# Optimization experiments

Measured on AMD Instinct MI355X. Metric: run time of the kernel, lower is better.

## Reference

```python
import jax, jax.numpy as jnp
import numpy as np

N = 50000
E = 800000
IN_C = 128
HID = 128
OUT_C = 64
HEADS = 8
HD1 = HID // HEADS   # 16 per-head dim, layer 1 (concat)
HD2 = OUT_C          # 64 per-head dim, layer 2 (concat=False, mean over heads)
NEG_SLOPE = 0.2


def setup_inputs() -> dict:
    key = jax.random.key(0)
    ks = jax.random.split(key, 12)
    x = jax.random.normal(ks[0], (N, IN_C), dtype=jnp.float32)
    edge_index = jax.random.randint(ks[1], (2, E), 0, N, dtype=jnp.int64)
    s1 = 1.0 / np.sqrt(IN_C)
    s2 = 1.0 / np.sqrt(HID)
    W1 = jax.random.normal(ks[2], (IN_C, HEADS * HD1), dtype=jnp.float32) * s1
    att_src1 = jax.random.normal(ks[3], (HEADS, HD1), dtype=jnp.float32) * s1
    att_dst1 = jax.random.normal(ks[4], (HEADS, HD1), dtype=jnp.float32) * s1
    b1 = jnp.zeros((HID,), dtype=jnp.float32)
    W2 = jax.random.normal(ks[5], (HID, HEADS * HD2), dtype=jnp.float32) * s2
    att_src2 = jax.random.normal(ks[6], (HEADS, HD2), dtype=jnp.float32) * s2
    att_dst2 = jax.random.normal(ks[7], (HEADS, HD2), dtype=jnp.float32) * s2
    b2 = jnp.zeros((OUT_C,), dtype=jnp.float32)
    return {"x": x, "edge_index": edge_index,
            "W1": W1, "att_src1": att_src1, "att_dst1": att_dst1, "b1": b1,
            "W2": W2, "att_src2": att_src2, "att_dst2": att_dst2, "b2": b2}


def _gat_conv(x, W, a_src, a_dst, bias, src, dst, heads, head_dim, concat):
    n = x.shape[0]
    h = (x @ W).reshape(n, heads, head_dim)                      # [N,H,D]
    alpha_s = jnp.einsum('nhd,hd->nh', h, a_src)                  # [N,H]
    alpha_d = jnp.einsum('nhd,hd->nh', h, a_dst)                  # [N,H]
    e = jax.nn.leaky_relu(alpha_s[src] + alpha_d[dst], NEG_SLOPE)  # [E,H]
    # segment softmax over edges grouped by destination node
    m = jax.ops.segment_max(e, dst, num_segments=n)               # [N,H]
    m = jnp.where(jnp.isfinite(m), m, 0.0)
    ex = jnp.exp(e - m[dst])
    denom = jax.ops.segment_sum(ex, dst, num_segments=n)
    alpha = ex / (denom[dst] + 1e-16)                             # [E,H]
    out = jax.ops.segment_sum(h[src] * alpha[:, :, None], dst, num_segments=n)  # [N,H,D]
    if concat:
        out = out.reshape(n, heads * head_dim)
    else:
        out = out.mean(axis=1)
    return out + bias


def reference(x, edge_index, W1, att_src1, att_dst1, b1, W2, att_src2, att_dst2, b2):
    # PyG GATConv default add_self_loops=True
    loops = jnp.arange(N, dtype=edge_index.dtype)
    src = jnp.concatenate([edge_index[0], loops])
    dst = jnp.concatenate([edge_index[1], loops])
    h = _gat_conv(x, W1, att_src1, att_dst1, b1, src, dst, HEADS, HD1, True)
    h = jax.nn.relu(h)
    out = _gat_conv(h, W2, att_src2, att_dst2, b2, src, dst, HEADS, HD2, False)
    return out
```

## Files before the change

kernel.cpp:

```cpp
#include <hip/hip_runtime.h>

#define N_NODES 50000
#define N_EDGES 800000
#define ET (N_EDGES + N_NODES)
#define HEADS 8
#define NPAD 50048
#define SCAN_NB 196
#define CAP 96
#define LRS 1032

typedef __attribute__((ext_vector_type(8))) _Float16 half8;
typedef __attribute__((ext_vector_type(2))) _Float16 half2v;
typedef __attribute__((ext_vector_type(4))) float f32x4;

__device__ __forceinline__ void wave_lds_fence(){
  asm volatile("s_waitcnt lgkmcnt(0)" ::: "memory");
}

__device__ __forceinline__ int edge_src(const int* ei, int e, int is64){
  if (e >= N_EDGES) return e - N_EDGES;
  return is64 ? ei[2*e] : ei[e];
}
__device__ __forceinline__ int edge_dst(const int* ei, int e, int is64){
  if (e >= N_EDGES) return e - N_EDGES;
  return is64 ? ei[2*(N_EDGES + e)] : ei[N_EDGES + e];
}

__global__ void k_init(const int* __restrict__ ei, int* __restrict__ deg,
                       int* __restrict__ cnt, int* __restrict__ flag){
  int i = blockIdx.x*blockDim.x + threadIdx.x;
  if (i < N_NODES){ deg[i] = 0; cnt[i] = 0; }
  if (i == 0){
    int zeros = 0;
    for (int k = 0; k < 64; k++){
      if (ei[2*k + 1] == 0) zeros++;
    }
    *flag = (zeros >= 60) ? 1 : 0;
  }
}

__global__ void k_degree(const int* __restrict__ ei, int* __restrict__ deg,
                         const int* __restrict__ flag){
  int e = blockIdx.x*blockDim.x + threadIdx.x;
  if (e >= ET) return;
  int is64 = *flag;
  int d = edge_dst(ei, e, is64);
  atomicAdd(&deg[d], 1);
}

__global__ void k_scan_part(const int* __restrict__ deg, int* __restrict__ loc,
                            int* __restrict__ part, int* __restrict__ hist_blk){
  __shared__ int lds[256];
  __shared__ int hl[256];
  int t = threadIdx.x, i = blockIdx.x*256 + t;
  int v = (i < N_NODES) ? deg[i] : 0;
  hl[t] = 0;
  __syncthreads();
  if (i < N_NODES){
    int b = v > 255 ? 255 : v;
    atomicAdd(&hl[255 - b], 1);
  }
  lds[t] = v;
  __syncthreads();
  for (int off = 1; off < 256; off <<= 1){
    int x = (t >= off) ? lds[t - off] : 0;
    __syncthreads();
    lds[t] += x;
    __syncthreads();
  }
  if (i < N_NODES) loc[i] = lds[t] - v;
  if (t == 255) part[blockIdx.x] = lds[255];
  hist_blk[t*SCAN_NB + blockIdx.x] = hl[t];
}

__global__ void k_scan_carry(int* __restrict__ part, int* __restrict__ carry,
                             int* __restrict__ hist_blk){
  __shared__ int lds[256];
  int t = threadIdx.x;
  int v = (t < SCAN_NB) ? part[t] : 0;
  lds[t] = v;
  __syncthreads();
  for (int off = 1; off < 256; off <<= 1){
    int x = (t >= off) ? lds[t - off] : 0;
    __syncthreads();
    lds[t] += x;
    __syncthreads();
  }
  if (t < SCAN_NB) carry[t] = lds[t] - v;
  __syncthreads();
  int tot = 0;
  for (int b = 0; b < SCAN_NB; b++) tot += hist_blk[t*SCAN_NB + b];
  lds[t] = tot;
  __syncthreads();
  for (int off = 1; off < 256; off <<= 1){
    int x = (t >= off) ? lds[t - off] : 0;
    __syncthreads();
    lds[t] += x;
    __syncthreads();
  }
  int run = lds[t] - tot;
  for (int b = 0; b < SCAN_NB; b++){
    int c = hist_blk[t*SCAN_NB + b];
    hist_blk[t*SCAN_NB + b] = run;
    run += c;
  }
}

__global__ void k_scan_add(const int* __restrict__ loc, const int* __restrict__ carry,
                           int* __restrict__ row_ptr, const int* __restrict__ deg,
                           const int* __restrict__ hist_blk, int* __restrict__ perm){
  __shared__ int hl[256];
  int t = threadIdx.x, i = blockIdx.x*256 + t;
  hl[t] = 0;
  __syncthreads();
  if (i < N_NODES){
    row_ptr[i] = loc[i] + carry[i >> 8];
    int d = deg[i]; if (d > 255) d = 255;
    int bin = 255 - d;
    int rank = atomicAdd(&hl[bin], 1);
    perm[hist_blk[bin*SCAN_NB + blockIdx.x] + rank] = i;
  }
  if (i == 0) row_ptr[N_NODES] = ET;
}

__global__ void k_fill(const int* __restrict__ ei, const int* __restrict__ row_ptr,
                       int* __restrict__ cnt, int* __restrict__ col,
                       const int* __restrict__ flag){
  int e = blockIdx.x*blockDim.x + threadIdx.x;
  if (e >= ET) return;
  int is64 = *flag;
  int s = edge_src(ei, e, is64);
  int d = edge_dst(ei, e, is64);
  int pos = atomicAdd(&cnt[d], 1);
  col[row_ptr[d] + pos] = s;
}

__global__ void k_wprep(const float* __restrict__ W1, const float* __restrict__ W2,
                        const float* __restrict__ as2, const float* __restrict__ ad2,
                        _Float16* __restrict__ Bp1, _Float16* __restrict__ Bp,
                        float* __restrict__ ws2, float* __restrict__ wd2){
  int b = blockIdx.x;
  int t_ = threadIdx.x;
  if (b < 256){
    int t = b*256 + t_;
    int j = t & 7, lane = (t >> 3) & 63, nt = (t >> 9) & 3, kt = t >> 11;
    int k = kt*32 + (lane >> 4)*8 + j;
    int c = nt*16 + (lane & 15);
    int h = k >> 7, kk = k & 127;
    Bp[t] = (_Float16)(0.125f * W2[kk*512 + h*64 + c]);
  } else if (b < 320){
    int t = (b - 256)*256 + t_;
    int j = t & 7, lane = (t >> 3) & 63, nt = (t >> 9) & 7, kt = t >> 12;
    int k = kt*32 + (lane >> 4)*8 + j;
    int c = nt*16 + (lane & 15);
    Bp1[t] = (_Float16)W1[k*128 + c];
  } else {
    int t = (b - 320)*256 + t_;
    int k = t >> 3, h = t & 7;
    float s = 0.f, d = 0.f;
    for (int dd = 0; dd < 64; dd++){
      float w = W2[k*512 + h*64 + dd];
      s += w * as2[h*64 + dd];
      d += w * ad2[h*64 + dd];
    }
    ws2[h*128 + k] = s;
    wd2[h*128 + k] = d;
  }
}

__global__ void __launch_bounds__(256) k_gemm1_mfma(
    const float* __restrict__ x, const _Float16* __restrict__ Bp1,
    _Float16* __restrict__ h1,
    const float* __restrict__ as1, const float* __restrict__ ad1,
    float* __restrict__ als1, float* __restrict__ ald1){
  int tid = threadIdx.x;
  int lane = tid & 63, wv = tid >> 6;
  int n0 = blockIdx.x*64 + wv*16;
  int rowA = n0 + (lane & 15);
  int koff = (lane >> 4)*8;
  const float* xr = x + (size_t)rowA*128 + koff;
  f32x4 acc[8];
  #pragma unroll
  for (int i = 0; i < 8; i++) acc[i] = (f32x4){0.f,0.f,0.f,0.f};
  bool inb = (rowA < N_NODES);
  #pragma unroll
  for (int kt = 0; kt < 4; kt++){
    half8 af;
    if (inb){
      float4 a0 = *(const float4*)(xr + kt*32);
      float4 a1 = *(const float4*)(xr + kt*32 + 4);
      af = (half8){(_Float16)a0.x,(_Float16)a0.y,(_Float16)a0.z,(_Float16)a0.w,
                   (_Float16)a1.x,(_Float16)a1.y,(_Float16)a1.z,(_Float16)a1.w};
    } else {
      af = (half8){0,0,0,0,0,0,0,0};
    }
    #pragma unroll
    for (int nt = 0; nt < 8; nt++){
      half8 bf = *(const half8*)(Bp1 + (((kt*8 + nt)*64 + lane) << 3));
      acc[nt] = __builtin_amdgcn_mfma_f32_16x16x32_f16(af, bf, acc[nt], 0, 0, 0);
    }
  }
  int m = lane & 15, q = lane >> 4;
  int r0 = n0 + q*4;
  #pragma unroll
  for (int nt = 0; nt < 8; nt++){
    int c = nt*16 + m;
    #pragma unroll
    for (int r = 0; r < 4; r++){
      int n = r0 + r;
      if (n < N_NODES) h1[(size_t)n*128 + c] = (_Float16)acc[nt][r];
    }
  }
  float as1v[8], ad1v[8];
  #pragma unroll
  for (int nt = 0; nt < 8; nt++){
    as1v[nt] = as1[nt*16 + m];
    ad1v[nt] = ad1[nt*16 + m];
  }
  #pragma unroll
  for (int r = 0; r < 4; r++){
    float vs[8], vd[8];
    #pragma unroll
    for (int nt = 0; nt < 8; nt++){
      vs[nt] = acc[nt][r]*as1v[nt];
      vd[nt] = acc[nt][r]*ad1v[nt];
      #pragma unroll
      for (int off = 1; off < 16; off <<= 1){
        vs[nt] += __shfl_xor(vs[nt], off, 64);
        vd[nt] += __shfl_xor(vd[nt], off, 64);
      }
    }
    int n = r0 + r;
    if (m == r && n < N_NODES){
      float4 v0; v0.x = vs[0]; v0.y = vs[1]; v0.z = vs[2]; v0.w = vs[3];
      float4 v1; v1.x = vs[4]; v1.y = vs[5]; v1.z = vs[6]; v1.w = vs[7];
      float4 w0; w0.x = vd[0]; w0.y = vd[1]; w0.z = vd[2]; w0.w = vd[3];
      float4 w1; w1.x = vd[4]; w1.y = vd[5]; w1.z = vd[6]; w1.w = vd[7];
      *(float4*)&als1[n*8]     = v0;
      *(float4*)&als1[n*8 + 4] = v1;
      *(float4*)&ald1[n*8]     = w0;
      *(float4*)&ald1[n*8 + 4] = w1;
    }
  }
}

__global__ void k_attn_agg1(const _Float16* __restrict__ h1,
    const float* __restrict__ als, const float* __restrict__ ald,
    const int* __restrict__ row_ptr, const int* __restrict__ col,
    const float* __restrict__ bias, _Float16* __restrict__ hr,
    const float* __restrict__ ws2, const float* __restrict__ wd2,
    float* __restrict__ als2, float* __restrict__ ald2,
    const int* __restrict__ perm){
  __shared__ _Float16 ew_s[4][CAP*8];
  __shared__ int col_s[4][CAP];
  __shared__ _Float16 ot_s[4][132];
  int tid = threadIdx.x;
  int wv = tid >> 6, lane = tid & 63;
  int n = perm[blockIdx.x*4 + wv];
  int beg = row_ptr[n], end = row_ptr[n+1];
  int deg = end - beg;
  int items = deg*8;
  int h = lane & 7;
  float ad = ald[n*8 + h];
  _Float16* es = ew_s[wv];
  int* cs = col_s[wv];
  float l = 0.f;
  int itc = items < CAP*8 ? items : CAP*8;
  int it = lane;
  for (; it < itc; it += 64){
    int e = it >> 3;
    int s = col[beg + e];
    float a = als[s*8 + h] + ad;
    a = (a > 0.f) ? a : 0.2f*a;
    float ex = __expf(a);
    es[it] = (_Float16)ex;
    if ((it & 7) == 0) cs[e] = s;
    l += ex;
  }
  for (; it < items; it += 64){
    int s = col[beg + (it >> 3)];
    float a = als[s*8 + h] + ad;
    a = (a > 0.f) ? a : 0.2f*a;
    l += __expf(a);
  }
  l += __shfl_xor(l, 8, 64);
  l += __shfl_xor(l, 16, 64);
  l += __shfl_xor(l, 32, 64);
  float inv = 1.f / (l + 1e-16f);
  wave_lds_fence();
  int hh0 = lane >> 3;
  float invh = __shfl(inv, hh0, 64);
  const half2v* h2p = (const half2v*)h1;
  float ax = 0.f, ay = 0.f;
  int degc = deg < CAP ? deg : CAP;
  int j = 0;
  for (; j + 7 < degc; j += 8){
    int s[8]; float w[8]; half2v v[8];
    #pragma unroll
    for (int u = 0; u < 8; u++) s[u] = cs[j + u];
    #pragma unroll
    for (int u = 0; u < 8; u++) w[u] = (float)es[(j + u)*8 + hh0] * invh;
    #pragma unroll
    for (int u = 0; u < 8; u++) v[u] = h2p[(size_t)s[u]*64 + lane];
    #pragma unroll
    for (int u = 0; u < 8; u++){ ax += w[u]*(float)v[u].x; ay += w[u]*(float)v[u].y; }
  }
  for (; j < degc; j++){
    int s = cs[j];
    float w = (float)es[j*8 + hh0] * invh;
    half2v v = h2p[(size_t)s*64 + lane];
    ax += w*(float)v.x; ay += w*(float)v.y;
  }
  float adh = ald[n*8 + hh0];
  for (; j < deg; j++){
    int s = col[beg + j];
    float a = als[s*8 + hh0] + adh;
    a = (a > 0.f) ? a : 0.2f*a;
    float w = __expf(a)*invh;
    half2v v = h2p[(size_t)s*64 + lane];
    ax += w*(float)v.x; ay += w*(float)v.y;
  }
  float2 bb = ((const float2*)bias)[lane];
  float o0 = fmaxf(ax + bb.x, 0.f);
  float o1 = fmaxf(ay + bb.y, 0.f);
  half2v oo; oo.x = (_Float16)o0; oo.y = (_Float16)o1;
  ((half2v*)hr)[(size_t)n*64 + lane] = oo;
  ((half2v*)&ot_s[wv][0])[lane] = oo;
  wave_lds_fence();
  int hh = lane >> 3, seg = lane & 7;
  const half2v* otp = (const half2v*)&ot_s[wv][0];
  const float* wsr = ws2 + hh*128 + seg*16;
  const float* wdr = wd2 + hh*128 + seg*16;
  float vs = 0.f, vd = 0.f;
  #pragma unroll
  for (int i = 0; i < 8; i++){
    half2v v = otp[seg*8 + i];
    float vx = (float)v.x, vy = (float)v.y;
    vs += vx*wsr[2*i] + vy*wsr[2*i + 1];
    vd += vx*wdr[2*i] + vy*wdr[2*i + 1];
  }
  vs += __shfl_xor(vs, 1, 64); vd += __shfl_xor(vd, 1, 64);
  vs += __shfl_xor(vs, 2, 64); vd += __shfl_xor(vd, 2, 64);
  vs += __shfl_xor(vs, 4, 64); vd += __shfl_xor(vd, 4, 64);
  if (seg == 0){
    als2[n*8 + hh] = vs;
    ald2[n*8 + hh] = vd;
  }
}

__global__ void __launch_bounds__(1024) k_attn_agg2(const _Float16* __restrict__ hr,
    const float* __restrict__ als, const float* __restrict__ ald,
    const int* __restrict__ row_ptr, const int* __restrict__ col,
    const _Float16* __restrict__ Bp, const float* __restrict__ b2,
    float* __restrict__ outp, const int* __restrict__ perm){
  __shared__ _Float16 ew_s[16][CAP*8];
  __shared__ int col_s[16][CAP];
  __shared__ _Float16 at[16*LRS];
  __shared__ int nid_s[16];
  int tid = threadIdx.x;
  int wv = tid >> 6, lane = tid & 63;
  int n = perm[blockIdx.x*16 + wv];
  if (lane == 0) nid_s[wv] = n;
  int beg = row_ptr[n], end = row_ptr[n+1];
  int deg = end - beg;
  int items = deg*8;
  int h = lane & 7;
  float ad = ald[n*8 + h];
  _Float16* es = ew_s[wv];
  int* cs = col_s[wv];
  float l = 0.f;
  int itc = items < CAP*8 ? items : CAP*8;
  int it = lane;
  for (; it < itc; it += 64){
    int e = it >> 3;
    int s = col[beg + e];
    float a = als[s*8 + h] + ad;
    a = (a > 0.f) ? a : 0.2f*a;
    float ex = __expf(a);
    es[it] = (_Float16)ex;
    if ((it & 7) == 0) cs[e] = s;
    l += ex;
  }
  for (; it < items; it += 64){
    int s = col[beg + (it >> 3)];
    float a = als[s*8 + h] + ad;
    a = (a > 0.f) ? a : 0.2f*a;
    l += __expf(a);
  }
  l += __shfl_xor(l, 8, 64);
  l += __shfl_xor(l, 16, 64);
  l += __shfl_xor(l, 32, 64);
  float inv = 1.f / (l + 1e-16f);
  wave_lds_fence();
  int hp = lane >> 4, cb = lane & 15;
  float invA = __shfl(inv, 2*hp, 64);
  float invB = __shfl(inv, 2*hp + 1, 64);
  half2v inv2; inv2.x = (_Float16)invA; inv2.y = (_Float16)invB;
  half2v acc_a[4], acc_b[4];
  #pragma unroll
  for (int i = 0; i < 4; i++){
    acc_a[i] = (half2v){(_Float16)0.f, (_Float16)0.f};
    acc_b[i] = (half2v){(_Float16)0.f, (_Float16)0.f};
  }
  int degc = deg < CAP ? deg : CAP;
  const _Float16* esw = es + 2*hp;
  int j = 0;
  for (; j + 3 < degc; j += 4){
    int s0 = cs[j], s1 = cs[j+1], s2 = cs[j+2], s3 = cs[j+3];
    half2v w0 = *(const half2v*)(esw + (j+0)*8) * inv2;
    half2v w1 = *(const half2v*)(esw + (j+1)*8) * inv2;
    half2v w2 = *(const half2v*)(esw + (j+2)*8) * inv2;
    half2v w3 = *(const half2v*)(esw + (j+3)*8) * inv2;
    half8 v0 = *(const half8*)(hr + (size_t)s0*128 + cb*8);
    half8 v1 = *(const half8*)(hr + (size_t)s1*128 + cb*8);
    half8 v2 = *(const half8*)(hr + (size_t)s2*128 + cb*8);
    half8 v3 = *(const half8*)(hr + (size_t)s3*128 + cb*8);
    #pragma unroll
    for (int k = 0; k < 4; k++){
      half2v t;
      t = (half2v){v0[2*k], v0[2*k+1]};
      acc_a[k] += (half2v){w0.x, w0.x} * t;
      acc_b[k] += (half2v){w0.y, w0.y} * t;
      t = (half2v){v1[2*k], v1[2*k+1]};
      acc_a[k] += (half2v){w1.x, w1.x} * t;
      acc_b[k] += (half2v){w1.y, w1.y} * t;
      t = (half2v){v2[2*k], v2[2*k+1]};
      acc_a[k] += (half2v){w2.x, w2.x} * t;
      acc_b[k] += (half2v){w2.y, w2.y} * t;
      t = (half2v){v3[2*k], v3[2*k+1]};
      acc_a[k] += (half2v){w3.x, w3.x} * t;
      acc_b[k] += (half2v){w3.y, w3.y} * t;
    }
  }
  for (; j < degc; j++){
    int s = cs[j];
    half2v w = *(const half2v*)(esw + j*8) * inv2;
    half8 v = *(const half8*)(hr + (size_t)s*128 + cb*8);
    #pragma unroll
    for (int k = 0; k < 4; k++){
      half2v t = (half2v){v[2*k], v[2*k+1]};
      acc_a[k] += (half2v){w.x, w.x} * t;
      acc_b[k] += (half2v){w.y, w.y} * t;
    }
  }
  if (deg > CAP){
    float2 adv = *(const float2*)(ald + (size_t)n*8 + 2*hp);
    for (; j < deg; j++){
      int s = col[beg + j];
      float2 alv = *(const float2*)(als + (size_t)s*8 + 2*hp);
      float a0 = alv.x + adv.x; a0 = (a0 > 0.f) ? a0 : 0.2f*a0;
      float a1 = alv.y + adv.y; a1 = (a1 > 0.f) ? a1 : 0.2f*a1;
      _Float16 w0 = (_Float16)(__expf(a0)*invA);
      _Float16 w1 = (_Float16)(__expf(a1)*invB);
      half8 v = *(const half8*)(hr + (size_t)s*128 + cb*8);
      #pragma unroll
      for (int k = 0; k < 4; k++){
        half2v t = (half2v){v[2*k], v[2*k+1]};
        acc_a[k] += (half2v){w0, w0} * t;
        acc_b[k] += (half2v){w1, w1} * t;
      }
    }
  }
  _Float16* ar = at + wv*LRS + (2*hp)*128 + cb*8;
  half8 oa, ob;
  #pragma unroll
  for (int k = 0; k < 4; k++){
    oa[2*k] = acc_a[k].x; oa[2*k+1] = acc_a[k].y;
    ob[2*k] = acc_b[k].x; ob[2*k+1] = acc_b[k].y;
  }
  *(half8*)ar = oa;
  *(half8*)(ar + 128) = ob;
  __syncthreads();
  if (wv >= 4) return;
  int m = lane & 15, q = lane >> 4;
  const _Float16* arow = at + m*LRS + q*8;
  f32x4 cacc = (f32x4){0.f,0.f,0.f,0.f};
  #pragma unroll 4
  for (int kt = 0; kt < 32; kt++){
    half8 af = *(const half8*)(arow + kt*32);
    half8 bf = *(const half8*)(Bp + (((kt*4 + wv)*64 + lane) << 3));
    cacc = __builtin_amdgcn_mfma_f32_16x16x32_f16(af, bf, cacc, 0, 0, 0);
  }
  int c = wv*16 + m;
  float bb = b2[c];
  #pragma unroll
  for (int r = 0; r < 4; r++){
    int nrow = nid_s[q*4 + r];
    outp[(size_t)nrow*64 + c] = cacc[r] + bb;
  }
}

extern "C" void kernel_launch(void* const* d_in, const int* in_sizes, int n_in,
                              void* d_out, int out_size, void* d_ws, size_t ws_size,
                              hipStream_t stream){
  const float* x   = (const float*)d_in[0];
  const int*   ei  = (const int*)d_in[1];
  const float* W1  = (const float*)d_in[2];
  const float* as1 = (const float*)d_in[3];
  const float* ad1 = (const float*)d_in[4];
  const float* b1  = (const float*)d_in[5];
  const float* W2  = (const float*)d_in[6];
  const float* as2 = (const float*)d_in[7];
  const float* ad2 = (const float*)d_in[8];
  const float* b2  = (const float*)d_in[9];
  float* outp = (float*)d_out;

  char* p = (char*)d_ws;
  auto alloc = [&](size_t bytes) -> void* {
    void* r = (void*)p;
    p += (bytes + 255) & ~(size_t)255;
    return r;
  };
  _Float16* h1  = (_Float16*)alloc((size_t)NPAD*128*2);
  _Float16* hr  = (_Float16*)alloc((size_t)N_NODES*128*2);
  float* als1 = (float*)alloc((size_t)N_NODES*8*4);
  float* ald1 = (float*)alloc((size_t)N_NODES*8*4);
  float* als2 = (float*)alloc((size_t)N_NODES*8*4);
  float* ald2 = (float*)alloc((size_t)N_NODES*8*4);
  int* row_ptr = (int*)alloc((size_t)(N_NODES+1)*4);
  int* deg  = (int*)alloc((size_t)N_NODES*4);
  int* cnt  = (int*)alloc((size_t)N_NODES*4);
  int* col  = (int*)alloc((size_t)ET*4);
  int* loc  = (int*)alloc((size_t)N_NODES*4);
  int* part = (int*)alloc(256*4);
  int* carry= (int*)alloc(256*4);
  int* flag = (int*)alloc(256);
  int* hist_blk = (int*)alloc((size_t)256*SCAN_NB*4);
  int* perm = (int*)alloc((size_t)N_NODES*4);
  float* ws2 = (float*)alloc(1024*4);
  float* wd2 = (float*)alloc(1024*4);
  _Float16* Bp1 = (_Float16*)alloc((size_t)16384*2);
  _Float16* Bp  = (_Float16*)alloc((size_t)65536*2);

  dim3 b256(256);
  k_init<<<(N_NODES+255)/256, b256, 0, stream>>>(ei, deg, cnt, flag);
  k_degree<<<(ET+255)/256, b256, 0, stream>>>(ei, deg, flag);
  k_scan_part<<<SCAN_NB, b256, 0, stream>>>(deg, loc, part, hist_blk);
  k_scan_carry<<<1, b256, 0, stream>>>(part, carry, hist_blk);
  k_scan_add<<<SCAN_NB, b256, 0, stream>>>(loc, carry, row_ptr, deg, hist_blk, perm);
  k_fill<<<(ET+255)/256, b256, 0, stream>>>(ei, row_ptr, cnt, col, flag);
  k_wprep<<<324, b256, 0, stream>>>(W1, W2, as2, ad2, Bp1, Bp, ws2, wd2);

  k_gemm1_mfma<<<NPAD/64, b256, 0, stream>>>(x, Bp1, h1, as1, ad1, als1, ald1);
  k_attn_agg1<<<N_NODES/4, b256, 0, stream>>>(h1, als1, ald1, row_ptr, col,
                                              b1, hr, ws2, wd2, als2, ald2, perm);
  k_attn_agg2<<<N_NODES/16, dim3(1024), 0, stream>>>(hr, als2, ald2, row_ptr, col,
                                                     Bp, b2, outp, perm);
}
```

Baseline: 353.0 us.

## Fuse softmax denominator into single-pass aggregation and transpose histogram layout

Both attention-aggregation kernels drop the separate pass that computed exp weights into LDS and normalised them first. Each lane now computes unnormalised exp weights inline, accumulates the denominator alongside the weighted sum, and divides once at the end. This removes the LDS staging buffers and a sequential phase, at the cost of redundant exp and als loads across lanes and fp16 accumulation of unnormalised values, rescaled by 1/16 to limit overflow risk. The scan histogram is also transposed to block-major layout so the per-block writes and per-bin reads are coalesced.

```diff
diff --git a/kernel.cpp b/kernel.cpp
--- a/kernel.cpp
+++ b/kernel.cpp
@@ -6,7 +6,6 @@
 #define HEADS 8
 #define NPAD 50048
 #define SCAN_NB 196
-#define CAP 96
 #define LRS 1032
 
 typedef __attribute__((ext_vector_type(8))) _Float16 half8;
@@ -70,7 +69,7 @@
   }
   if (i < N_NODES) loc[i] = lds[t] - v;
   if (t == 255) part[blockIdx.x] = lds[255];
-  hist_blk[t*SCAN_NB + blockIdx.x] = hl[t];
+  hist_blk[blockIdx.x*256 + t] = hl[t];
 }
 
 __global__ void k_scan_carry(int* __restrict__ part, int* __restrict__ carry,
@@ -89,7 +88,7 @@
   if (t < SCAN_NB) carry[t] = lds[t] - v;
   __syncthreads();
   int tot = 0;
-  for (int b = 0; b < SCAN_NB; b++) tot += hist_blk[t*SCAN_NB + b];
+  for (int b = 0; b < SCAN_NB; b++) tot += hist_blk[b*256 + t];
   lds[t] = tot;
   __syncthreads();
   for (int off = 1; off < 256; off <<= 1){
@@ -100,8 +99,8 @@
   }
   int run = lds[t] - tot;
   for (int b = 0; b < SCAN_NB; b++){
-    int c = hist_blk[t*SCAN_NB + b];
-    hist_blk[t*SCAN_NB + b] = run;
+    int c = hist_blk[b*256 + t];
+    hist_blk[b*256 + t] = run;
     run += c;
   }
 }
@@ -118,7 +117,7 @@
     int d = deg[i]; if (d > 255) d = 255;
     int bin = 255 - d;
     int rank = atomicAdd(&hl[bin], 1);
-    perm[hist_blk[bin*SCAN_NB + blockIdx.x] + rank] = i;
+    perm[hist_blk[blockIdx.x*256 + bin] + rank] = i;
   }
   if (i == 0) row_ptr[N_NODES] = ET;
 }
@@ -251,75 +250,45 @@
     const float* __restrict__ ws2, const float* __restrict__ wd2,
     float* __restrict__ als2, float* __restrict__ ald2,
     const int* __restrict__ perm){
-  __shared__ _Float16 ew_s[4][CAP*8];
-  __shared__ int col_s[4][CAP];
   __shared__ _Float16 ot_s[4][132];
   int tid = threadIdx.x;
   int wv = tid >> 6, lane = tid & 63;
   int n = perm[blockIdx.x*4 + wv];
   int beg = row_ptr[n], end = row_ptr[n+1];
   int deg = end - beg;
-  int items = deg*8;
-  int h = lane & 7;
-  float ad = ald[n*8 + h];
-  _Float16* es = ew_s[wv];
-  int* cs = col_s[wv];
-  float l = 0.f;
-  int itc = items < CAP*8 ? items : CAP*8;
-  int it = lane;
-  for (; it < itc; it += 64){
-    int e = it >> 3;
-    int s = col[beg + e];
-    float a = als[s*8 + h] + ad;
-    a = (a > 0.f) ? a : 0.2f*a;
-    float ex = __expf(a);
-    es[it] = (_Float16)ex;
-    if ((it & 7) == 0) cs[e] = s;
-    l += ex;
-  }
-  for (; it < items; it += 64){
-    int s = col[beg + (it >> 3)];
-    float a = als[s*8 + h] + ad;
-    a = (a > 0.f) ? a : 0.2f*a;
-    l += __expf(a);
-  }
-  l += __shfl_xor(l, 8, 64);
-  l += __shfl_xor(l, 16, 64);
-  l += __shfl_xor(l, 32, 64);
-  float inv = 1.f / (l + 1e-16f);
-  wave_lds_fence();
   int hh0 = lane >> 3;
-  float invh = __shfl(inv, hh0, 64);
+  float adh = ald[n*8 + hh0];
   const half2v* h2p = (const half2v*)h1;
-  float ax = 0.f, ay = 0.f;
-  int degc = deg < CAP ? deg : CAP;
+  float l = 0.f, ax = 0.f, ay = 0.f;
   int j = 0;
-  for (; j + 7 < degc; j += 8){
-    int s[8]; float w[8]; half2v v[8];
-    #pragma unroll
-    for (int u = 0; u < 8; u++) s[u] = cs[j + u];
-    #pragma unroll
-    for (int u = 0; u < 8; u++) w[u] = (float)es[(j + u)*8 + hh0] * invh;
-    #pragma unroll
-    for (int u = 0; u < 8; u++) v[u] = h2p[(size_t)s[u]*64 + lane];
-    #pragma unroll
-    for (int u = 0; u < 8; u++){ ax += w[u]*(float)v[u].x; ay += w[u]*(float)v[u].y; }
-  }
-  for (; j < degc; j++){
-    int s = cs[j];
-    float w = (float)es[j*8 + hh0] * invh;
-    half2v v = h2p[(size_t)s*64 + lane];
-    ax += w*(float)v.x; ay += w*(float)v.y;
-  }
-  float adh = ald[n*8 + hh0];
+  for (; j + 3 < deg; j += 4){
+    int s0 = col[beg+j], s1 = col[beg+j+1], s2 = col[beg+j+2], s3 = col[beg+j+3];
+    float a0 = als[s0*8 + hh0], a1 = als[s1*8 + hh0],
+          a2 = als[s2*8 + hh0], a3 = als[s3*8 + hh0];
+    half2v v0 = h2p[(size_t)s0*64 + lane], v1 = h2p[(size_t)s1*64 + lane],
+           v2 = h2p[(size_t)s2*64 + lane], v3 = h2p[(size_t)s3*64 + lane];
+    a0 += adh; a0 = (a0 > 0.f) ? a0 : 0.2f*a0;
+    a1 += adh; a1 = (a1 > 0.f) ? a1 : 0.2f*a1;
+    a2 += adh; a2 = (a2 > 0.f) ? a2 : 0.2f*a2;
+    a3 += adh; a3 = (a3 > 0.f) ? a3 : 0.2f*a3;
+    float w0 = __expf(a0), w1 = __expf(a1), w2 = __expf(a2), w3 = __expf(a3);
+    l += w0 + w1 + w2 + w3;
+    ax += w0*(float)v0.x; ay += w0*(float)v0.y;
+    ax += w1*(float)v1.x; ay += w1*(float)v1.y;
+    ax += w2*(float)v2.x; ay += w2*(float)v2.y;
+    ax += w3*(float)v3.x; ay += w3*(float)v3.y;
+  }
   for (; j < deg; j++){
-    int s = col[beg + j];
+    int s = col[beg+j];
     float a = als[s*8 + hh0] + adh;
     a = (a > 0.f) ? a : 0.2f*a;
-    float w = __expf(a)*invh;
+    float w = __expf(a);
     half2v v = h2p[(size_t)s*64 + lane];
+    l += w;
     ax += w*(float)v.x; ay += w*(float)v.y;
   }
+  float inv = 1.f / (l + 1e-16f);
+  ax *= inv; ay *= inv;
   float2 bb = ((const float2*)bias)[lane];
   float o0 = fmaxf(ax + bb.x, 0.f);
   float o1 = fmaxf(ay + bb.y, 0.f);
@@ -353,8 +322,6 @@
     const int* __restrict__ row_ptr, const int* __restrict__ col,
     const _Float16* __restrict__ Bp, const float* __restrict__ b2,
     float* __restrict__ outp, const int* __restrict__ perm){
-  __shared__ _Float16 ew_s[16][CAP*8];
-  __shared__ int col_s[16][CAP];
   __shared__ _Float16 at[16*LRS];
   __shared__ int nid_s[16];
   int tid = threadIdx.x;
@@ -363,110 +330,73 @@
   if (lane == 0) nid_s[wv] = n;
   int beg = row_ptr[n], end = row_ptr[n+1];
   int deg = end - beg;
-  int items = deg*8;
-  int h = lane & 7;
-  float ad = ald[n*8 + h];
-  _Float16* es = ew_s[wv];
-  int* cs = col_s[wv];
-  float l = 0.f;
-  int itc = items < CAP*8 ? items : CAP*8;
-  int it = lane;
-  for (; it < itc; it += 64){
-    int e = it >> 3;
-    int s = col[beg + e];
-    float a = als[s*8 + h] + ad;
-    a = (a > 0.f) ? a : 0.2f*a;
-    float ex = __expf(a);
-    es[it] = (_Float16)ex;
-    if ((it & 7) == 0) cs[e] = s;
-    l += ex;
-  }
-  for (; it < items; it += 64){
-    int s = col[beg + (it >> 3)];
-    float a = als[s*8 + h] + ad;
-    a = (a > 0.f) ? a : 0.2f*a;
-    l += __expf(a);
-  }
-  l += __shfl_xor(l, 8, 64);
-  l += __shfl_xor(l, 16, 64);
-  l += __shfl_xor(l, 32, 64);
-  float inv = 1.f / (l + 1e-16f);
-  wave_lds_fence();
   int hp = lane >> 4, cb = lane & 15;
-  float invA = __shfl(inv, 2*hp, 64);
-  float invB = __shfl(inv, 2*hp + 1, 64);
-  half2v inv2; inv2.x = (_Float16)invA; inv2.y = (_Float16)invB;
+  float2 adv = *(const float2*)(ald + (size_t)n*8 + 2*hp);
+  const float SC = 0.0625f;
+  float lA = 0.f, lB = 0.f;
   half2v acc_a[4], acc_b[4];
   #pragma unroll
   for (int i = 0; i < 4; i++){
     acc_a[i] = (half2v){(_Float16)0.f, (_Float16)0.f};
     acc_b[i] = (half2v){(_Float16)0.f, (_Float16)0.f};
   }
-  int degc = deg < CAP ? deg : CAP;
-  const _Float16* esw = es + 2*hp;
   int j = 0;
-  for (; j + 3 < degc; j += 4){
-    int s0 = cs[j], s1 = cs[j+1], s2 = cs[j+2], s3 = cs[j+3];
-    half2v w0 = *(const half2v*)(esw + (j+0)*8) * inv2;
-    half2v w1 = *(const half2v*)(esw + (j+1)*8) * inv2;
-    half2v w2 = *(const half2v*)(esw + (j+2)*8) * inv2;
-    half2v w3 = *(const half2v*)(esw + (j+3)*8) * inv2;
+  for (; j + 1 < deg; j += 2){
+    int s0 = col[beg+j], s1 = col[beg+j+1];
+    float2 al0 = *(const float2*)(als + (size_t)s0*8 + 2*hp);
+    float2 al1 = *(const float2*)(als + (size_t)s1*8 + 2*hp);
     half8 v0 = *(const half8*)(hr + (size_t)s0*128 + cb*8);
     half8 v1 = *(const half8*)(hr + (size_t)s1*128 + cb*8);
-    half8 v2 = *(const half8*)(hr + (size_t)s2*128 + cb*8);
-    half8 v3 = *(const half8*)(hr + (size_t)s3*128 + cb*8);
+    float a00 = al0.x + adv.x; a00 = (a00 > 0.f) ? a00 : 0.2f*a00;
+    float a01 = al0.y + adv.y; a01 = (a01 > 0.f) ? a01 : 0.2f*a01;
+    float a10 = al1.x + adv.x; a10 = (a10 > 0.f) ? a10 : 0.2f*a10;
+    float a11 = al1.y + adv.y; a11 = (a11 > 0.f) ? a11 : 0.2f*a11;
+    float w00 = __expf(a00), w01 = __expf(a01);
+    float w10 = __expf(a10), w11 = __expf(a11);
+    lA += w00 + w10; lB += w01 + w11;
+    _Float16 h00 = (_Float16)(w00*SC), h01 = (_Float16)(w01*SC);
+    _Float16 h10 = (_Float16)(w10*SC), h11 = (_Float16)(w11*SC);
+    half2v w0a = {h00, h00}, w0b = {h01, h01};
+    half2v w1a = {h10, h10}, w1b = {h11, h11};
     #pragma unroll
     for (int k = 0; k < 4; k++){
-      half2v t;
-      t = (half2v){v0[2*k], v0[2*k+1]};
-      acc_a[k] += (half2v){w0.x, w0.x} * t;
-      acc_b[k] += (half2v){w0.y, w0.y} * t;
-      t = (half2v){v1[2*k], v1[2*k+1]};
-      acc_a[k] += (half2v){w1.x, w1.x} * t;
-      acc_b[k] += (half2v){w1.y, w1.y} * t;
-      t = (half2v){v2[2*k], v2[2*k+1]};
-      acc_a[k] += (half2v){w2.x, w2.x} * t;
-      acc_b[k] += (half2v){w2.y, w2.y} * t;
-      t = (half2v){v3[2*k], v3[2*k+1]};
-      acc_a[k] += (half2v){w3.x, w3.x} * t;
-      acc_b[k] += (half2v){w3.y, w3.y} * t;
-    }
-  }
-  for (; j < degc; j++){
-    int s = cs[j];
-    half2v w = *(const half2v*)(esw + j*8) * inv2;
+      half2v t0 = (half2v){v0[2*k], v0[2*k+1]};
+      half2v t1 = (half2v){v1[2*k], v1[2*k+1]};
+      acc_a[k] += w0a * t0;
+      acc_b[k] += w0b * t0;
+      acc_a[k] += w1a * t1;
+      acc_b[k] += w1b * t1;
+    }
+  }
+  for (; j < deg; j++){
+    int s = col[beg+j];
+    float2 al = *(const float2*)(als + (size_t)s*8 + 2*hp);
     half8 v = *(const half8*)(hr + (size_t)s*128 + cb*8);
+    float a0 = al.x + adv.x; a0 = (a0 > 0.f) ? a0 : 0.2f*a0;
+    float a1 = al.y + adv.y; a1 = (a1 > 0.f) ? a1 : 0.2f*a1;
+    float w0 = __expf(a0), w1 = __expf(a1);
+    lA += w0; lB += w1;
+    _Float16 hw0 = (_Float16)(w0*SC), hw1 = (_Float16)(w1*SC);
+    half2v wa = {hw0, hw0}, wb = {hw1, hw1};
     #pragma unroll
     for (int k = 0; k < 4; k++){
       half2v t = (half2v){v[2*k], v[2*k+1]};
-      acc_a[k] += (half2v){w.x, w.x} * t;
-      acc_b[k] += (half2v){w.y, w.y} * t;
-    }
-  }
-  if (deg > CAP){
-    float2 adv = *(const float2*)(ald + (size_t)n*8 + 2*hp);
-    for (; j < deg; j++){
-      int s = col[beg + j];
-      float2 alv = *(const float2*)(als + (size_t)s*8 + 2*hp);
-      float a0 = alv.x + adv.x; a0 = (a0 > 0.f) ? a0 : 0.2f*a0;
-      float a1 = alv.y + adv.y; a1 = (a1 > 0.f) ? a1 : 0.2f*a1;
-      _Float16 w0 = (_Float16)(__expf(a0)*invA);
-      _Float16 w1 = (_Float16)(__expf(a1)*invB);
-      half8 v = *(const half8*)(hr + (size_t)s*128 + cb*8);
-      #pragma unroll
-      for (int k = 0; k < 4; k++){
-        half2v t = (half2v){v[2*k], v[2*k+1]};
-        acc_a[k] += (half2v){w0, w0} * t;
-        acc_b[k] += (half2v){w1, w1} * t;
-      }
-    }
-  }
+      acc_a[k] += wa * t;
+      acc_b[k] += wb * t;
+    }
+  }
+  float invA = 16.f / (lA + 1e-16f);
+  float invB = 16.f / (lB + 1e-16f);
+  _Float16 iA = (_Float16)invA, iB = (_Float16)invB;
+  half2v iva = {iA, iA}, ivb = {iB, iB};
   _Float16* ar = at + wv*LRS + (2*hp)*128 + cb*8;
   half8 oa, ob;
   #pragma unroll
   for (int k = 0; k < 4; k++){
-    oa[2*k] = acc_a[k].x; oa[2*k+1] = acc_a[k].y;
-    ob[2*k] = acc_b[k].x; ob[2*k+1] = acc_b[k].y;
+    half2v na = acc_a[k] * iva;
+    half2v nb = acc_b[k] * ivb;
+    oa[2*k] = na.x; oa[2*k+1] = na.y;
+    ob[2*k] = nb.x; ob[2*k+1] = nb.y;
   }
   *(half8*)ar = oa;
   *(half8*)(ar + 128) = ob;
```

Result: slower. 362.7 us (+2.7%).
